# Optimization experiments

Measured on AMD Instinct MI355X. Metric: run time of the kernel, lower is better.

## Reference

```python
import jax, jax.numpy as jnp
import numpy as np

N_HEAD = 4
D_K = 512 // N_HEAD  # 128
PAD = 5  # (kernel 11 - 1) // 2, sanm_shift=0 -> symmetric 'same' padding
EPS = 1e-5


def layer_norm(x, w, b):
    m = jnp.mean(x, axis=-1, keepdims=True)
    v = jnp.mean(jnp.square(x - m), axis=-1, keepdims=True)
    return (x - m) * jax.lax.rsqrt(v + EPS) * w + b


def setup_inputs() -> dict:
    key = jax.random.key(0)
    ks = jax.random.split(key, 8)
    B, T, D = 64, 218, 512
    s = 0.05
    return {
        "x": jax.random.normal(ks[0], (B, T, D), jnp.float32),
        "masks": jnp.ones((B, T), jnp.float32),
        "ln0_w": jax.random.uniform(ks[1], (D,), jnp.float32, 0.9, 1.1),
        "ln0_b": jnp.zeros((D,), jnp.float32),
        "ln1_w": jax.random.uniform(ks[2], (D,), jnp.float32, 0.9, 1.1),
        "ln1_b": jnp.zeros((D,), jnp.float32),
        "qkv_w": jax.random.normal(ks[3], (D, 3 * D), jnp.float32) * s,
        "qkv_b": jnp.zeros((3 * D,), jnp.float32),
        "out_w": jax.random.normal(ks[4], (D, D), jnp.float32) * s,
        "out_b": jnp.zeros((D,), jnp.float32),
        "fsmn_w": jax.random.normal(ks[5], (D, D, 11), jnp.float32) * s,
        "w1": jax.random.normal(ks[6], (D, 4 * D), jnp.float32) * s,
        "b1": jnp.zeros((4 * D,), jnp.float32),
        "w2": jax.random.normal(ks[7], (4 * D, D), jnp.float32) * s,
        "b2": jnp.zeros((D,), jnp.float32),
    }


def encoder_layer(x, masks, ln0_w, ln0_b, ln1_w, ln1_b, qkv_w, qkv_b,
                  out_w, out_b, fsmn_w, w1, b1, w2, b2):
    B, T, D = x.shape
    m = masks[..., None]  # (B,T,1)

    # ---- self_attn_sanm block ----
    residual = x
    h = layer_norm(x, ln0_w, ln0_b)
    qkv = h @ qkv_w + qkv_b                      # (B,T,3D)
    q, k, v = jnp.split(qkv, 3, axis=-1)         # each (B,T,D)

    # FSMN memory branch on (masked) v: Conv1d(512,512,11), 'same' padding
    vm = v * m
    # torch conv weight (out,in,k) -> jax 'WIO' kernel (k,in,out)
    kern = jnp.transpose(fsmn_w, (2, 1, 0))
    fsmn = jax.lax.conv_general_dilated(
        vm, kern, window_strides=(1,), padding=[(PAD, PAD)],
        dimension_numbers=("NWC", "WIO", "NWC"))
    fsmn = (fsmn + vm) * m                       # (B,T,D)

    # multi-head attention
    def heads(t):  # (B,T,D) -> (B,H,T,dk)
        return t.reshape(B, T, N_HEAD, D_K).transpose(0, 2, 1, 3)
    qh, kh, vh = heads(q), heads(k), heads(v)
    scores = jnp.einsum("bhqd,bhkd->bhqk", qh, kh) / np.sqrt(D_K)
    neg = jnp.finfo(scores.dtype).min
    scores = jnp.where(masks[:, None, None, :] > 0, scores, neg)
    attn = jax.nn.softmax(scores, axis=-1)
    ctx = jnp.einsum("bhqk,bhkd->bhqd", attn, vh)
    ctx = ctx.transpose(0, 2, 1, 3).reshape(B, T, D)
    att_out = ctx @ out_w + out_b + fsmn
    x = residual + att_out

    # ---- feed-forward block (512 -> 2048 -> 512, relu) ----
    residual = x
    h = layer_norm(x, ln1_w, ln1_b)
    ffn = jax.nn.relu(h @ w1 + b1) @ w2 + b2
    return residual + ffn


def reference(x, masks, ln0_w, ln0_b, ln1_w, ln1_b, qkv_w, qkv_b,
              out_w, out_b, fsmn_w, w1, b1, w2, b2):
    return encoder_layer(x, masks, ln0_w, ln0_b, ln1_w, ln1_b,
                         qkv_w, qkv_b, out_w, out_b, fsmn_w, w1, b1, w2, b2)
```

## Files before the change

kernel.cpp:

```cpp
#include <hip/hip_runtime.h>
#include <cstdint>

#define B_   64
#define T_   218
#define TP_  228
#define D_   512
#define M_   13952
#define MT_  109
#define H_   4
#define DK_  128
#define PW_  224
#define N3_  1536
#define DFF_ 2048
#define KC_  5632
#define KH_  2816

typedef unsigned short u16;
using short8 = __attribute__((ext_vector_type(8))) short;
using f32x4  = __attribute__((ext_vector_type(4))) float;

__device__ __forceinline__ float b2f(u16 u) {
  union { float f; uint32_t i; } v; v.i = ((uint32_t)u) << 16; return v.f;
}
__device__ __forceinline__ u16 f2b(float f) {
  union { float f; uint32_t i; } v; v.f = f;
  uint32_t r = v.i + 0x7fffu + ((v.i >> 16) & 1u);
  return (u16)(r >> 16);
}
union U8 { uint4 v; u16 u[8]; };

__device__ __forceinline__ void gll16(const u16* g, u16* l) {
  __builtin_amdgcn_global_load_lds(
      (const __attribute__((address_space(1))) unsigned int*)g,
      (__attribute__((address_space(3))) unsigned int*)l, 16, 0, 0);
}

template<int MODE>
__global__ __launch_bounds__(256, 2)
void gemm_u(const u16* __restrict__ A, int sA, const u16* __restrict__ Bt, int sB,
            const float* __restrict__ bias, const u16* __restrict__ convb,
            const u16* __restrict__ vmp, u16* __restrict__ vmout,
            const float* __restrict__ add_f, void* __restrict__ outp,
            int N, int K, int ntc, const float* __restrict__ masks)
{
  __shared__ u16 As[128 * 32];
  __shared__ u16 Bs[128 * 32];

  int mt, nt, zb = 0;
  if (MODE == 4) {
    const int j = blockIdx.x & 7;
    nt = j & 3; zb = j >> 2;
    mt = blockIdx.x >> 3;
  } else {
    const int xcd = blockIdx.x & 7;
    const int lin = blockIdx.x >> 3;
    nt = lin % ntc;
    mt = xcd + 8 * (lin / ntc);
    if (mt >= MT_) return;
  }
  const int m0 = mt * 128, n0 = nt * 128;

  const int tid = threadIdx.x, lane = tid & 63, w = tid >> 6;
  const int wm = (w >> 1) * 64, wn = (w & 1) * 64;
  const int l15 = lane & 15, qd = lane >> 4;

  const int rl = lane >> 2, ce = (lane & 3) * 8;
  const int r0 = m0 + w * 16 + rl, r1 = r0 + 64;
  size_t aoff0, aoff1, bkoff = 0;
  if (MODE == 4) {
    const int b0r = r0 / T_, t0r = r0 - b0r * T_;
    const int b1r = r1 / T_, t1r = r1 - b1r * T_;
    aoff0 = ((size_t)b0r * TP_ + t0r) * D_ + (size_t)zb * KH_;
    aoff1 = ((size_t)b1r * TP_ + t1r) * D_ + (size_t)zb * KH_;
    bkoff = (size_t)zb * KH_;
  } else {
    aoff0 = (size_t)r0 * sA;
    aoff1 = (size_t)r1 * sA;
  }
  const u16* ag0 = A + aoff0 + ce;
  const u16* ag1 = A + aoff1 + ce;
  const u16* bg0 = Bt + (size_t)(n0 + w * 16 + rl) * sB + bkoff + ce;
  const u16* bg1 = bg0 + (size_t)64 * sB;
  u16* lA0 = As + w * 512;
  u16* lA1 = As + 2048 + w * 512;
  u16* lB0 = Bs + w * 512;
  u16* lB1 = Bs + 2048 + w * 512;

  const f32x4 z4 = {0.f, 0.f, 0.f, 0.f};
  f32x4 acc[4][4];
#pragma unroll
  for (int i = 0; i < 4; i++)
#pragma unroll
    for (int j = 0; j < 4; j++) acc[i][j] = z4;

  for (int k0 = 0; k0 < K; k0 += 32) {
    __syncthreads();
    gll16(ag0 + k0, lA0);
    gll16(ag1 + k0, lA1);
    gll16(bg0 + k0, lB0);
    gll16(bg1 + k0, lB1);
    __syncthreads();
    short8 af[4], bf[4];
#pragma unroll
    for (int mi = 0; mi < 4; mi++) af[mi] = *(const short8*)&As[(wm + mi * 16 + l15) * 32 + qd * 8];
#pragma unroll
    for (int ni = 0; ni < 4; ni++) bf[ni] = *(const short8*)&Bs[(wn + ni * 16 + l15) * 32 + qd * 8];
#pragma unroll
    for (int mi = 0; mi < 4; mi++)
#pragma unroll
      for (int ni = 0; ni < 4; ni++)
        acc[mi][ni] = __builtin_amdgcn_mfma_f32_16x16x32_bf16(af[mi], bf[ni], acc[mi][ni], 0, 0, 0);
  }

#pragma unroll
  for (int ni = 0; ni < 4; ni++) {
    const int c = n0 + wn + ni * 16 + l15;
    const float bv = (MODE == 4) ? 0.f : bias[c];
#pragma unroll
    for (int mi = 0; mi < 4; mi++) {
#pragma unroll
      for (int rg = 0; rg < 4; rg++) {
        const int r = m0 + wm + mi * 16 + qd * 4 + rg;
        float v = acc[mi][ni][rg] + bv;
        if (MODE == 0) {
          ((u16*)outp)[(size_t)r * N + c] = f2b(v);
          if (c >= 1024) {
            const int b = r / T_, t = r - b * T_;
            vmout[((size_t)b * TP_ + t + 5) * D_ + (c - 1024)] = f2b(v * masks[r]);
          }
        } else if (MODE == 1) {
          const size_t idx = (size_t)r * N + c;
          const int b = r / T_, t = r - b * T_;
          const float m  = masks[r];
          const float cv = b2f(convb[idx]) + b2f(convb[idx + (size_t)M_ * 512]);
          const float vm = b2f(vmp[((size_t)b * TP_ + t + 5) * D_ + c]);
          ((float*)outp)[idx] = v + (cv + vm) * m + add_f[idx];
        } else if (MODE == 2) {
          ((u16*)outp)[(size_t)r * N + c] = f2b(fmaxf(v, 0.f));
        } else if (MODE == 3) {
          const size_t idx = (size_t)r * N + c;
          ((float*)outp)[idx] = v + add_f[idx];
        } else {
          ((u16*)outp)[(size_t)zb * ((size_t)M_ * 512) + (size_t)r * N + c] = f2b(v);
        }
      }
    }
  }
}

__global__ __launch_bounds__(256, 2)
void attn_fused(const u16* __restrict__ qkv, const float* __restrict__ masks,
                u16* __restrict__ ctx)
{
  __shared__ u16 smem[29696];
  __shared__ float red0[4][64];
  __shared__ float red1[4][64];
  u16* Qs = smem;
  u16* Ks = smem + 64 * 136;
  u16* Ps = smem;
  u16* Vs = smem + 64 * 232;

  const int tid = threadIdx.x, lane = tid & 63, w = tid >> 6;
  const int l15 = lane & 15, qd = lane >> 4;
  const int bh = blockIdx.y, b = bh >> 2, h = bh & 3;
  const int q0 = blockIdx.x * 64;
  const uint4 uz = make_uint4(0, 0, 0, 0);

#pragma unroll
  for (int i = 0; i < 4; i++) {
    const int ch = tid + i * 256;
    const int row = ch >> 4, cg = (ch & 15) * 8;
    const int t = q0 + row;
    uint4 v = uz;
    if (t < T_) v = *(const uint4*)(qkv + ((size_t)b * T_ + t) * N3_ + h * DK_ + cg);
    *(uint4*)&Qs[row * 136 + cg] = v;
  }

  const f32x4 z4 = {0.f, 0.f, 0.f, 0.f};
  f32x4 acc[4][4];
#pragma unroll
  for (int i = 0; i < 4; i++)
#pragma unroll
    for (int j = 0; j < 4; j++) acc[i][j] = z4;

#pragma unroll
  for (int kc = 0; kc < 4; kc++) {
    __syncthreads();
#pragma unroll
    for (int i = 0; i < 4; i++) {
      const int ch = tid + i * 256;
      const int row = ch >> 4, cg = (ch & 15) * 8;
      const int t = kc * 64 + row;
      uint4 v = uz;
      if (t < T_) v = *(const uint4*)(qkv + ((size_t)b * T_ + t) * N3_ + D_ + h * DK_ + cg);
      *(uint4*)&Ks[row * 136 + cg] = v;
    }
    __syncthreads();
#pragma unroll
    for (int ks = 0; ks < 4; ks++) {
      short8 bf = *(const short8*)&Ks[(w * 16 + l15) * 136 + ks * 32 + qd * 8];
#pragma unroll
      for (int mi = 0; mi < 4; mi++) {
        short8 af = *(const short8*)&Qs[(mi * 16 + l15) * 136 + ks * 32 + qd * 8];
        acc[kc][mi] = __builtin_amdgcn_mfma_f32_16x16x32_bf16(af, bf, acc[kc][mi], 0, 0, 0);
      }
    }
  }

  const float scale = 0.08838834764831845f;
  const int colb = w * 16 + l15;
  bool valid[4];
#pragma unroll
  for (int kc = 0; kc < 4; kc++) {
    const int col = kc * 64 + colb;
    valid[kc] = (col < T_) && (masks[b * T_ + col] > 0.f);
  }

  float mx[4][4];
#pragma unroll
  for (int mi = 0; mi < 4; mi++)
#pragma unroll
    for (int rg = 0; rg < 4; rg++) {
      float m = -1e30f;
#pragma unroll
      for (int kc = 0; kc < 4; kc++)
        if (valid[kc]) m = fmaxf(m, acc[kc][mi][rg] * scale);
      for (int d = 1; d < 16; d <<= 1) m = fmaxf(m, __shfl_xor(m, d, 64));
      mx[mi][rg] = m;
    }
  if (l15 == 0) {
#pragma unroll
    for (int mi = 0; mi < 4; mi++)
#pragma unroll
      for (int rg = 0; rg < 4; rg++) red0[w][mi * 16 + qd * 4 + rg] = mx[mi][rg];
  }
  __syncthreads();
#pragma unroll
  for (int mi = 0; mi < 4; mi++)
#pragma unroll
    for (int rg = 0; rg < 4; rg++) {
      const int r = mi * 16 + qd * 4 + rg;
      mx[mi][rg] = fmaxf(fmaxf(red0[0][r], red0[1][r]), fmaxf(red0[2][r], red0[3][r]));
    }
  float sm[4][4];
#pragma unroll
  for (int mi = 0; mi < 4; mi++)
#pragma unroll
    for (int rg = 0; rg < 4; rg++) {
      float s = 0.f;
#pragma unroll
      for (int kc = 0; kc < 4; kc++)
        if (valid[kc]) s += __expf(acc[kc][mi][rg] * scale - mx[mi][rg]);
      for (int d = 1; d < 16; d <<= 1) s += __shfl_xor(s, d, 64);
      sm[mi][rg] = s;
    }
  if (l15 == 0) {
#pragma unroll
    for (int mi = 0; mi < 4; mi++)
#pragma unroll
      for (int rg = 0; rg < 4; rg++) red1[w][mi * 16 + qd * 4 + rg] = sm[mi][rg];
  }
  __syncthreads();
#pragma unroll
  for (int mi = 0; mi < 4; mi++)
#pragma unroll
    for (int rg = 0; rg < 4; rg++) {
      const int r = mi * 16 + qd * 4 + rg;
      const float inv = 1.f / (red1[0][r] + red1[1][r] + red1[2][r] + red1[3][r]);
#pragma unroll
      for (int kc = 0; kc < 4; kc++) {
        const int col = kc * 64 + colb;
        if (col < PW_) {
          const float p = valid[kc] ? __expf(acc[kc][mi][rg] * scale - mx[mi][rg]) * inv : 0.f;
          Ps[r * 232 + col] = f2b(p);
        }
      }
    }

  const int kvg = tid >> 4, dg = tid & 15;
#pragma unroll
  for (int half = 0; half < 2; ++half) {
    __syncthreads();
#pragma unroll
    for (int r = 0; r < 14; ++r) {
      const int kv = r * 16 + kvg;
      ushort4 vv = make_ushort4(0, 0, 0, 0);
      if (kv < T_)
        vv = *(const ushort4*)(qkv + ((size_t)b * T_ + kv) * N3_ + 1024 + h * DK_ + half * 64 + dg * 4);
      Vs[(dg * 4 + 0) * 232 + kv] = vv.x;
      Vs[(dg * 4 + 1) * 232 + kv] = vv.y;
      Vs[(dg * 4 + 2) * 232 + kv] = vv.z;
      Vs[(dg * 4 + 3) * 232 + kv] = vv.w;
    }
    __syncthreads();
    f32x4 a2[4] = {z4, z4, z4, z4};
#pragma unroll
    for (int k0 = 0; k0 < 7; ++k0) {
      short8 af = *(const short8*)&Ps[(w * 16 + l15) * 232 + k0 * 32 + qd * 8];
#pragma unroll
      for (int nt = 0; nt < 4; ++nt) {
        short8 bf = *(const short8*)&Vs[(nt * 16 + l15) * 232 + k0 * 32 + qd * 8];
        a2[nt] = __builtin_amdgcn_mfma_f32_16x16x32_bf16(af, bf, a2[nt], 0, 0, 0);
      }
    }
    const int tb = q0 + w * 16 + qd * 4;
#pragma unroll
    for (int nt = 0; nt < 4; ++nt) {
      const int d = h * DK_ + half * 64 + nt * 16 + l15;
#pragma unroll
      for (int rg = 0; rg < 4; ++rg) {
        const int tt = tb + rg;
        if (tt < T_) ctx[((size_t)b * T_ + tt) * D_ + d] = f2b(a2[nt][rg]);
      }
    }
  }
}

__global__ __launch_bounds__(256)
void ln_k(const float* __restrict__ x, const float* __restrict__ wgt,
          const float* __restrict__ bia, u16* __restrict__ outp)
{
  const int lane = threadIdx.x & 63, wv = threadIdx.x >> 6;
  const size_t row = (size_t)blockIdx.x * 4 + wv;
  const float* rp = x + row * D_ + lane * 8;
  float v[8], s = 0.f, s2 = 0.f;
  float4 r0 = *(const float4*)rp;
  float4 r1 = *(const float4*)(rp + 4);
  v[0] = r0.x; v[1] = r0.y; v[2] = r0.z; v[3] = r0.w;
  v[4] = r1.x; v[5] = r1.y; v[6] = r1.z; v[7] = r1.w;
#pragma unroll
  for (int i = 0; i < 8; i++) { s += v[i]; s2 += v[i] * v[i]; }
  for (int d = 1; d < 64; d <<= 1) { s += __shfl_xor(s, d, 64); s2 += __shfl_xor(s2, d, 64); }
  const float mean = s * (1.f / 512.f);
  const float var  = s2 * (1.f / 512.f) - mean * mean;
  const float rs   = rsqrtf(var + 1e-5f);
  float4 w0 = *(const float4*)(wgt + lane * 8);
  float4 w1 = *(const float4*)(wgt + lane * 8 + 4);
  float4 b0 = *(const float4*)(bia + lane * 8);
  float4 b1 = *(const float4*)(bia + lane * 8 + 4);
  const float wv8[8] = {w0.x, w0.y, w0.z, w0.w, w1.x, w1.y, w1.z, w1.w};
  const float bv8[8] = {b0.x, b0.y, b0.z, b0.w, b1.x, b1.y, b1.z, b1.w};
  U8 o;
#pragma unroll
  for (int i = 0; i < 8; i++)
    o.u[i] = f2b((v[i] - mean) * rs * wv8[i] + bv8[i]);
  *(uint4*)(outp + row * D_ + lane * 8) = o.v;
}

__global__ __launch_bounds__(256)
void prep_all(const float* __restrict__ qkv_w, const float* __restrict__ out_w,
              const float* __restrict__ w1, const float* __restrict__ w2,
              const float* __restrict__ fsmn_w,
              u16* __restrict__ qkv_wT, u16* __restrict__ out_wT,
              u16* __restrict__ w1T, u16* __restrict__ w2T,
              u16* __restrict__ fsmnW2, u16* __restrict__ vmpad)
{
  const int bid = blockIdx.x;
  if (bid < 3072) {
    const float* src; u16* dst; int K, N, tb;
    if (bid < 768)       { src = qkv_w; dst = qkv_wT; K = 512;  N = 1536; tb = bid; }
    else if (bid < 1024) { src = out_w; dst = out_wT; K = 512;  N = 512;  tb = bid - 768; }
    else if (bid < 2048) { src = w1;    dst = w1T;    K = 512;  N = 2048; tb = bid - 1024; }
    else                 { src = w2;    dst = w2T;    K = 2048; N = 512;  tb = bid - 2048; }
    const int ktiles = K / 32;
    const int k0 = (tb % ktiles) * 32, n0 = (tb / ktiles) * 32;
    __shared__ float tile[32][33];
    const int x = threadIdx.x & 31, y = threadIdx.x >> 5;
#pragma unroll
    for (int j = 0; j < 4; j++)
      tile[y + j * 8][x] = src[(size_t)(k0 + y + j * 8) * N + n0 + x];
    __syncthreads();
#pragma unroll
    for (int j = 0; j < 4; j++)
      dst[(size_t)(n0 + y + j * 8) * K + k0 + x] = f2b(tile[x][y + j * 8]);
  } else if (bid < 4096) {
    const int idx = (bid - 3072) * 256 + threadIdx.x;
    const int o = idx >> 9, i = idx & 511;
    const float* s = fsmn_w + (size_t)idx * 11;
#pragma unroll
    for (int tap = 0; tap < 11; ++tap)
      fsmnW2[(size_t)o * KC_ + tap * 512 + i] = f2b(s[tap]);
  } else {
    const int e8 = (bid - 4096) * 256 + threadIdx.x;
    const int e  = e8 * 8;
    const int c  = e & 511;
    const int pr = e >> 9;
    const int b  = pr / 10, j = pr % 10;
    const int row = (j < 5) ? j : (218 + j);
    *(uint4*)(vmpad + ((size_t)b * TP_ + row) * D_ + c) = make_uint4(0, 0, 0, 0);
  }
}

extern "C" void kernel_launch(void* const* d_in, const int* in_sizes, int n_in,
                              void* d_out, int out_size, void* d_ws, size_t ws_size,
                              hipStream_t stream)
{
  const float* x      = (const float*)d_in[0];
  const float* masks  = (const float*)d_in[1];
  const float* ln0_w  = (const float*)d_in[2];
  const float* ln0_b  = (const float*)d_in[3];
  const float* ln1_w  = (const float*)d_in[4];
  const float* ln1_b  = (const float*)d_in[5];
  const float* qkv_w  = (const float*)d_in[6];
  const float* qkv_b  = (const float*)d_in[7];
  const float* out_w  = (const float*)d_in[8];
  const float* out_b  = (const float*)d_in[9];
  const float* fsmn_w = (const float*)d_in[10];
  const float* w1     = (const float*)d_in[11];
  const float* b1     = (const float*)d_in[12];
  const float* w2     = (const float*)d_in[13];
  const float* b2     = (const float*)d_in[14];
  float* outp = (float*)d_out;
  u16* ws   = (u16*)d_ws;

  size_t off = 0;
  u16* qkv_wT = ws + off; off += (size_t)1536 * 512;
  u16* out_wT = ws + off; off += (size_t)512 * 512;
  u16* w1T    = ws + off; off += (size_t)2048 * 512;
  u16* w2T    = ws + off; off += (size_t)512 * 2048;
  u16* fsmnW2 = ws + off; off += (size_t)512 * KC_;
  u16* slotA  = ws + off; off += (size_t)M_ * 512;
  u16* qkvb   = ws + off; off += (size_t)M_ * 1536;
  u16* vmpad  = ws + off; off += (size_t)B_ * TP_ * 512;
  u16* regionX= ws + off;
  u16* convacc = regionX;
  u16* hid     = regionX;
  u16* h1      = qkvb;
  float* x1    = (float*)(qkvb + (size_t)M_ * 512);

  prep_all<<<4256, 256, 0, stream>>>(qkv_w, out_w, w1, w2, fsmn_w,
                                     qkv_wT, out_wT, w1T, w2T, fsmnW2, vmpad);
  ln_k<<<M_ / 4, 256, 0, stream>>>(x, ln0_w, ln0_b, slotA);
  gemm_u<0><<<8 * 14 * 12, 256, 0, stream>>>(
      slotA, 512, qkv_wT, 512, qkv_b, nullptr, nullptr, vmpad, nullptr, qkvb,
      1536, 512, 12, masks);
  gemm_u<4><<<MT_ * 8, 256, 0, stream>>>(
      vmpad, 0, fsmnW2, KC_, nullptr, nullptr, nullptr, nullptr, nullptr, convacc,
      512, KH_, 4, nullptr);
  attn_fused<<<dim3(4, 256), 256, 0, stream>>>(qkvb, masks, slotA);
  gemm_u<1><<<8 * 14 * 4, 256, 0, stream>>>(
      slotA, 512, out_wT, 512, out_b, convacc, vmpad, nullptr, x, x1,
      512, 512, 4, masks);
  ln_k<<<M_ / 4, 256, 0, stream>>>(x1, ln1_w, ln1_b, h1);
  gemm_u<2><<<8 * 14 * 16, 256, 0, stream>>>(
      h1, 512, w1T, 512, b1, nullptr, nullptr, nullptr, nullptr, hid,
      2048, 512, 16, nullptr);
  gemm_u<3><<<8 * 14 * 4, 256, 0, stream>>>(
      hid, 2048, w2T, 2048, b2, nullptr, nullptr, nullptr, x1, outp,
      512, 2048, 4, nullptr);
}
```

Before: 504.9 us.

## Replace im2col-style FSMN conv GEMM with tap-reusing shifted-window conv kernel

The FSMN depthwise-in-time conv previously ran as a split-K GEMM over an implicit im2col. Each of the two K halves reloaded padded rows per tap and wrote two bf16 partial outputs that the out-projection epilogue then summed with vm and mask. The new conv_gemm kernel loads a 288-row window of padded v once per 32-channel chunk and reuses it across all 11 taps by shifting LDS row offsets. It also fuses the residual vm add and masking into its epilogue, so the out-projection epilogue reads only one conv buffer. The cost is a larger LDS footprint (the 11-tap weight tile plus the window) and extra zero-padded tail rows in vmpad.

```diff
diff --git a/kernel.cpp b/kernel.cpp
--- a/kernel.cpp
+++ b/kernel.cpp
@@ -9,11 +9,9 @@
 #define MT_  109
 #define H_   4
 #define DK_  128
-#define PW_  224
 #define N3_  1536
 #define DFF_ 2048
 #define KC_  5632
-#define KH_  2816
 
 typedef unsigned short u16;
 using short8 = __attribute__((ext_vector_type(8))) short;
@@ -39,25 +37,18 @@
 __global__ __launch_bounds__(256, 2)
 void gemm_u(const u16* __restrict__ A, int sA, const u16* __restrict__ Bt, int sB,
             const float* __restrict__ bias, const u16* __restrict__ convb,
-            const u16* __restrict__ vmp, u16* __restrict__ vmout,
+            u16* __restrict__ vmout,
             const float* __restrict__ add_f, void* __restrict__ outp,
             int N, int K, int ntc, const float* __restrict__ masks)
 {
   __shared__ u16 As[128 * 32];
   __shared__ u16 Bs[128 * 32];
 
-  int mt, nt, zb = 0;
-  if (MODE == 4) {
-    const int j = blockIdx.x & 7;
-    nt = j & 3; zb = j >> 2;
-    mt = blockIdx.x >> 3;
-  } else {
-    const int xcd = blockIdx.x & 7;
-    const int lin = blockIdx.x >> 3;
-    nt = lin % ntc;
-    mt = xcd + 8 * (lin / ntc);
-    if (mt >= MT_) return;
-  }
+  const int xcd = blockIdx.x & 7;
+  const int lin = blockIdx.x >> 3;
+  const int nt = lin % ntc;
+  const int mt = xcd + 8 * (lin / ntc);
+  if (mt >= MT_) return;
   const int m0 = mt * 128, n0 = nt * 128;
 
   const int tid = threadIdx.x, lane = tid & 63, w = tid >> 6;
@@ -66,20 +57,9 @@
 
   const int rl = lane >> 2, ce = (lane & 3) * 8;
   const int r0 = m0 + w * 16 + rl, r1 = r0 + 64;
-  size_t aoff0, aoff1, bkoff = 0;
-  if (MODE == 4) {
-    const int b0r = r0 / T_, t0r = r0 - b0r * T_;
-    const int b1r = r1 / T_, t1r = r1 - b1r * T_;
-    aoff0 = ((size_t)b0r * TP_ + t0r) * D_ + (size_t)zb * KH_;
-    aoff1 = ((size_t)b1r * TP_ + t1r) * D_ + (size_t)zb * KH_;
-    bkoff = (size_t)zb * KH_;
-  } else {
-    aoff0 = (size_t)r0 * sA;
-    aoff1 = (size_t)r1 * sA;
-  }
-  const u16* ag0 = A + aoff0 + ce;
-  const u16* ag1 = A + aoff1 + ce;
-  const u16* bg0 = Bt + (size_t)(n0 + w * 16 + rl) * sB + bkoff + ce;
+  const u16* ag0 = A + (size_t)r0 * sA + ce;
+  const u16* ag1 = A + (size_t)r1 * sA + ce;
+  const u16* bg0 = Bt + (size_t)(n0 + w * 16 + rl) * sB + ce;
   const u16* bg1 = bg0 + (size_t)64 * sB;
   u16* lA0 = As + w * 512;
   u16* lA1 = As + 2048 + w * 512;
@@ -115,7 +95,7 @@
 #pragma unroll
   for (int ni = 0; ni < 4; ni++) {
     const int c = n0 + wn + ni * 16 + l15;
-    const float bv = (MODE == 4) ? 0.f : bias[c];
+    const float bv = bias[c];
 #pragma unroll
     for (int mi = 0; mi < 4; mi++) {
 #pragma unroll
@@ -130,18 +110,86 @@
           }
         } else if (MODE == 1) {
           const size_t idx = (size_t)r * N + c;
-          const int b = r / T_, t = r - b * T_;
-          const float m  = masks[r];
-          const float cv = b2f(convb[idx]) + b2f(convb[idx + (size_t)M_ * 512]);
-          const float vm = b2f(vmp[((size_t)b * TP_ + t + 5) * D_ + c]);
-          ((float*)outp)[idx] = v + (cv + vm) * m + add_f[idx];
+          ((float*)outp)[idx] = v + b2f(convb[idx]) + add_f[idx];
         } else if (MODE == 2) {
           ((u16*)outp)[(size_t)r * N + c] = f2b(fmaxf(v, 0.f));
-        } else if (MODE == 3) {
+        } else {
           const size_t idx = (size_t)r * N + c;
           ((float*)outp)[idx] = v + add_f[idx];
-        } else {
-          ((u16*)outp)[(size_t)zb * ((size_t)M_ * 512) + (size_t)r * N + c] = f2b(v);
+        }
+      }
+    }
+  }
+}
+
+__global__ __launch_bounds__(256, 2)
+void conv_gemm(const u16* __restrict__ vmpad, const u16* __restrict__ Wt,
+               const float* __restrict__ masks, u16* __restrict__ convb)
+{
+  __shared__ u16 As[288 * 32];
+  __shared__ u16 Bs[11 * 64 * 32];
+
+  const int nt = blockIdx.x & 7, mt = blockIdx.x >> 3;
+  const int m0 = mt * 256, n0 = nt * 64;
+  const int b0 = m0 / T_;
+  const int base = m0 + 10 * b0;
+
+  const int tid = threadIdx.x, lane = tid & 63, w = tid >> 6;
+  const int wm = (w >> 1) * 128, wn = (w & 1) * 32;
+  const int l15 = lane & 15, qd = lane >> 4;
+  const int rl = lane >> 2, ce = (lane & 3) * 8;
+
+  int arow[8];
+#pragma unroll
+  for (int mi = 0; mi < 8; mi++) {
+    const int mo = wm + mi * 16 + l15;
+    const int db = (m0 + mo) / T_ - b0;
+    arow[mi] = mo + 10 * db;
+  }
+
+  const f32x4 z4 = {0.f, 0.f, 0.f, 0.f};
+  f32x4 acc[8][2];
+#pragma unroll
+  for (int i = 0; i < 8; i++) { acc[i][0] = z4; acc[i][1] = z4; }
+
+  for (int kc = 0; kc < 16; kc++) {
+    const int kb = kc * 32;
+    __syncthreads();
+    for (int c = w; c < 18; c += 4)
+      gll16(vmpad + (size_t)(base + c * 16 + rl) * D_ + kb + ce, As + c * 512);
+    for (int c = w; c < 44; c += 4) {
+      const int tap = c >> 2, q = c & 3;
+      gll16(Wt + (size_t)(n0 + q * 16 + rl) * KC_ + tap * 512 + kb + ce,
+            Bs + c * 512);
+    }
+    __syncthreads();
+#pragma unroll
+    for (int tap = 0; tap < 11; tap++) {
+      short8 bf0 = *(const short8*)&Bs[tap * 2048 + (wn + l15) * 32 + qd * 8];
+      short8 bf1 = *(const short8*)&Bs[tap * 2048 + (wn + 16 + l15) * 32 + qd * 8];
+#pragma unroll
+      for (int mi = 0; mi < 8; mi++) {
+        short8 af = *(const short8*)&As[(arow[mi] + tap) * 32 + qd * 8];
+        acc[mi][0] = __builtin_amdgcn_mfma_f32_16x16x32_bf16(af, bf0, acc[mi][0], 0, 0, 0);
+        acc[mi][1] = __builtin_amdgcn_mfma_f32_16x16x32_bf16(af, bf1, acc[mi][1], 0, 0, 0);
+      }
+    }
+  }
+
+#pragma unroll
+  for (int mi = 0; mi < 8; mi++) {
+#pragma unroll
+    for (int rg = 0; rg < 4; rg++) {
+      const int r = m0 + wm + mi * 16 + qd * 4 + rg;
+      if (r < M_) {
+        const int b = r / T_;
+        const int vrow = r + 10 * b + 5;
+        const float m = masks[r];
+#pragma unroll
+        for (int ni = 0; ni < 2; ni++) {
+          const int c = n0 + wn + ni * 16 + l15;
+          const float vm = b2f(vmpad[(size_t)vrow * D_ + c]);
+          convb[(size_t)r * D_ + c] = f2b((acc[mi][ni][rg] + vm) * m);
         }
       }
     }
@@ -270,7 +318,7 @@
 #pragma unroll
       for (int kc = 0; kc < 4; kc++) {
         const int col = kc * 64 + colb;
-        if (col < PW_) {
+        if (col < 224) {
           const float p = valid[kc] ? __expf(acc[kc][mi][rg] * scale - mx[mi][rg]) * inv : 0.f;
           Ps[r * 232 + col] = f2b(p);
         }
@@ -385,9 +433,14 @@
     const int e  = e8 * 8;
     const int c  = e & 511;
     const int pr = e >> 9;
-    const int b  = pr / 10, j = pr % 10;
-    const int row = (j < 5) ? j : (218 + j);
-    *(uint4*)(vmpad + ((size_t)b * TP_ + row) * D_ + c) = make_uint4(0, 0, 0, 0);
+    int row;
+    if (pr < 640) {
+      const int b = pr / 10, j = pr % 10;
+      row = b * TP_ + ((j < 5) ? j : (218 + j));
+    } else {
+      row = B_ * TP_ + (pr - 640);
+    }
+    *(uint4*)(vmpad + (size_t)row * D_ + c) = make_uint4(0, 0, 0, 0);
   }
 }
 
@@ -421,31 +474,29 @@
   u16* fsmnW2 = ws + off; off += (size_t)512 * KC_;
   u16* slotA  = ws + off; off += (size_t)M_ * 512;
   u16* qkvb   = ws + off; off += (size_t)M_ * 1536;
-  u16* vmpad  = ws + off; off += (size_t)B_ * TP_ * 512;
+  u16* vmpad  = ws + off; off += (size_t)(B_ * TP_ + 320) * 512;
   u16* regionX= ws + off;
-  u16* convacc = regionX;
-  u16* hid     = regionX;
-  u16* h1      = qkvb;
-  float* x1    = (float*)(qkvb + (size_t)M_ * 512);
-
-  prep_all<<<4256, 256, 0, stream>>>(qkv_w, out_w, w1, w2, fsmn_w,
+  u16* convb  = regionX;
+  u16* hid    = regionX;
+  u16* h1     = qkvb;
+  float* x1   = (float*)(qkvb + (size_t)M_ * 512);
+
+  prep_all<<<4126, 256, 0, stream>>>(qkv_w, out_w, w1, w2, fsmn_w,
                                      qkv_wT, out_wT, w1T, w2T, fsmnW2, vmpad);
   ln_k<<<M_ / 4, 256, 0, stream>>>(x, ln0_w, ln0_b, slotA);
   gemm_u<0><<<8 * 14 * 12, 256, 0, stream>>>(
-      slotA, 512, qkv_wT, 512, qkv_b, nullptr, nullptr, vmpad, nullptr, qkvb,
+      slotA, 512, qkv_wT, 512, qkv_b, nullptr, vmpad, nullptr, qkvb,
       1536, 512, 12, masks);
-  gemm_u<4><<<MT_ * 8, 256, 0, stream>>>(
-      vmpad, 0, fsmnW2, KC_, nullptr, nullptr, nullptr, nullptr, nullptr, convacc,
-      512, KH_, 4, nullptr);
+  conv_gemm<<<55 * 8, 256, 0, stream>>>(vmpad, fsmnW2, masks, convb);
   attn_fused<<<dim3(4, 256), 256, 0, stream>>>(qkvb, masks, slotA);
   gemm_u<1><<<8 * 14 * 4, 256, 0, stream>>>(
-      slotA, 512, out_wT, 512, out_b, convacc, vmpad, nullptr, x, x1,
+      slotA, 512, out_wT, 512, out_b, convb, nullptr, x, x1,
       512, 512, 4, masks);
   ln_k<<<M_ / 4, 256, 0, stream>>>(x1, ln1_w, ln1_b, h1);
   gemm_u<2><<<8 * 14 * 16, 256, 0, stream>>>(
-      h1, 512, w1T, 512, b1, nullptr, nullptr, nullptr, nullptr, hid,
+      h1, 512, w1T, 512, b1, nullptr, nullptr, nullptr, hid,
       2048, 512, 16, nullptr);
   gemm_u<3><<<8 * 14 * 4, 256, 0, stream>>>(
-      hid, 2048, w2T, 2048, b2, nullptr, nullptr, nullptr, x1, outp,
+      hid, 2048, w2T, 2048, b2, nullptr, nullptr, x1, outp,
       512, 2048, 4, nullptr);
 }
```

Result: faster. 453.0 us (-10.3%).
